# Kernel tuning notes

Measured on AMD Instinct MI355X. Metric: run time of the kernel, lower is better.

Reference implementation:

```python
import jax, jax.numpy as jnp
import numpy as np

B, C, H, W = 32, 1536, 14, 14   # input is (B*4, C, H, W); joint -> (B, C, 2H, 2W)
CI = C // 2                     # non-local inter_channels
EPS = 1e-5


def conv1x1(x, w, b):
    # x: (b, cin, h, w); w: (cout, cin); b: (cout,)
    return jnp.einsum('bchw,oc->bohw', x, w) + b[None, :, None, None]


def maxpool2(x):
    b, c, h, w = x.shape
    return x.reshape(b, c, h // 2, 2, w // 2, 2).max(axis=(3, 5))


def setup_inputs():
    key = jax.random.key(0)
    ks = jax.random.split(key, 12)
    s = 0.02
    return {
        'x': jax.random.normal(ks[0], (B * 4, C, H, W), jnp.float32),
        'w_theta': jax.random.normal(ks[1], (CI, C), jnp.float32) * s,
        'b_theta': jnp.zeros((CI,), jnp.float32),
        'w_phi': jax.random.normal(ks[2], (CI, C), jnp.float32) * s,
        'b_phi': jnp.zeros((CI,), jnp.float32),
        'w_g': jax.random.normal(ks[3], (CI, C), jnp.float32) * s,
        'b_g': jnp.zeros((CI,), jnp.float32),
        'w_W': jax.random.normal(ks[4], (C, CI), jnp.float32) * s,
        'b_W': jnp.zeros((C,), jnp.float32),
        'bn_gamma': jax.random.normal(ks[5], (C,), jnp.float32) * 0.1 + 1.0,
        'bn_beta': jax.random.normal(ks[6], (C,), jnp.float32) * 0.1,
        'bn_mean': jax.random.normal(ks[7], (C,), jnp.float32) * 0.1,
        'bn_var': jnp.ones((C,), jnp.float32),
    }


def joint(x):
    # (B*4, C, H, W) -> (B, C, 2H, 2W): 4 views tiled in a 2x2 grid
    x4 = x.reshape(B, 4, C, H, W)
    top = jnp.concatenate([x4[:, 0], x4[:, 1]], axis=-1)   # (B, C, H, 2W)
    bot = jnp.concatenate([x4[:, 2], x4[:, 3]], axis=-1)
    return jnp.concatenate([top, bot], axis=-2)             # (B, C, 2H, 2W)


def reference(x, w_theta, b_theta, w_phi, b_phi, w_g, b_g, w_W, b_W,
              bn_gamma, bn_beta, bn_mean, bn_var):
    xj = joint(x)                                           # (B, C, Hj, Wj)
    b, c, hj, wj = xj.shape
    n = hj * wj                                             # 784 query positions

    theta = conv1x1(xj, w_theta, b_theta).reshape(b, CI, n)             # (B, CI, N)
    phi = maxpool2(conv1x1(xj, w_phi, b_phi)).reshape(b, CI, -1)        # (B, CI, N/4)
    g = maxpool2(conv1x1(xj, w_g, b_g)).reshape(b, CI, -1)              # (B, CI, N/4)

    f = jnp.einsum('bcn,bcm->bnm', theta, phi)              # (B, N, N/4)
    attn = jax.nn.softmax(f, axis=-1)
    y = jnp.einsum('bnm,bcm->bcn', attn, g)                 # (B, CI, N)
    y = y.reshape(b, CI, hj, wj)

    w_y = conv1x1(y, w_W, b_W)
    # BatchNorm (inference form)
    inv = jax.lax.rsqrt(bn_var + EPS)
    w_y = (w_y - bn_mean[None, :, None, None]) * (bn_gamma * inv)[None, :, None, None] \
          + bn_beta[None, :, None, None]
    return w_y + xj
```

## Files before the change

### kernel.cpp

```cpp
#include <hip/hip_runtime.h>
#include <hip/hip_bf16.h>

typedef __attribute__((ext_vector_type(8))) _Float16 f16x8;
typedef __attribute__((ext_vector_type(4))) float f32x4;
typedef __attribute__((ext_vector_type(4))) unsigned short us4;
typedef __attribute__((ext_vector_type(8))) unsigned short us8;

#define B_   32
#define C_   1536
#define CI_  768
#define N_   784
#define S_   196
#define MP_  224
#define MK_  196

__device__ __forceinline__ unsigned short f2h(float f) {
    _Float16 h = (_Float16)f;
    return __builtin_bit_cast(unsigned short, h);
}
__device__ __forceinline__ f32x4 mfma_f16(f16x8 a, f16x8 b, f32x4 c) {
    return __builtin_amdgcn_mfma_f32_16x16x32_f16(a, b, c, 0, 0, 0);
}
__device__ __forceinline__ void gl_lds16(const unsigned short* g, unsigned short* l) {
    __builtin_amdgcn_global_load_lds(
        (const __attribute__((address_space(1))) unsigned int*)g,
        (__attribute__((address_space(3))) unsigned int*)l, 16, 0, 0);
}

__device__ __forceinline__ void stage24(const unsigned short* Arow,
                                        const unsigned short* Brow,
                                        unsigned short* A_s, unsigned short* B_s,
                                        int k0, int stride,
                                        int wv, int l4r, int l4c_sw) {
    for (int c = wv; c < 24; c += 4) {
        if (c < 16) {
            gl_lds16(Arow + (size_t)(c * 16 + l4r) * stride + k0 + l4c_sw * 8,
                     A_s + c * 512);
        } else {
            int cb = c - 16;
            gl_lds16(Brow + (size_t)(cb * 16 + l4r) * stride + k0 + l4c_sw * 8,
                     B_s + cb * 512);
        }
    }
}

#define PIPE_WAIT_BARRIER()                                   \
    do {                                                      \
        asm volatile("s_waitcnt vmcnt(6)" ::: "memory");      \
        __builtin_amdgcn_s_barrier();                         \
        __builtin_amdgcn_sched_barrier(0);                    \
    } while (0)

__global__ __launch_bounds__(256) void k_cvt(const float* __restrict__ src,
                                             unsigned short* __restrict__ dst,
                                             int count4) {
    int idx = blockIdx.x * 256 + threadIdx.x;
    if (idx < count4) {
        f32x4 v = ((const f32x4*)src)[idx];
        us4 o;
        o[0] = f2h(v[0]); o[1] = f2h(v[1]); o[2] = f2h(v[2]); o[3] = f2h(v[3]);
        ((us4*)dst)[idx] = o;
    }
}

__global__ __launch_bounds__(256) void k_build_xjT(const float* __restrict__ x,
                                                   unsigned short* __restrict__ xjT) {
    __shared__ __align__(16) unsigned short lds[196 * 40];
    int c0 = blockIdx.x * 32;
    int b4 = blockIdx.y;
    int b = b4 >> 2, v = b4 & 3;
    int tid = threadIdx.x;
    const float* src = x + ((size_t)b4 * C_ + c0) * S_;
    for (int idx = tid; idx < 32 * 49; idx += 256) {
        int cl = idx / 49;
        int sq = idx - cl * 49;
        f32x4 val = *(const f32x4*)(src + (size_t)cl * S_ + sq * 4);
        int s = sq * 4;
        lds[(s + 0) * 40 + cl] = f2h(val[0]);
        lds[(s + 1) * 40 + cl] = f2h(val[1]);
        lds[(s + 2) * 40 + cl] = f2h(val[2]);
        lds[(s + 3) * 40 + cl] = f2h(val[3]);
    }
    __syncthreads();
    int rowbase = (v >> 1) * 14, colbase = (v & 1) * 14;
    for (int idx = tid; idx < 196 * 4; idx += 256) {
        int s = idx >> 2, ch = idx & 3;
        int hh = s / 14, ww = s - hh * 14;
        int n = (rowbase + hh) * 28 + colbase + ww;
        us8 val = *(const us8*)(&lds[s * 40 + ch * 8]);
        *(us8*)(xjT + ((size_t)b * N_ + n) * C_ + c0 + ch * 8) = val;
    }
}

__global__ __launch_bounds__(256) void k_bnprep(const float* __restrict__ bw,
                                                const float* __restrict__ gamma,
                                                const float* __restrict__ beta,
                                                const float* __restrict__ mean,
                                                const float* __restrict__ var,
                                                float* __restrict__ scale,
                                                float* __restrict__ shift) {
    int i = blockIdx.x * 256 + threadIdx.x;
    if (i < C_) {
        float sc = gamma[i] * rsqrtf(var[i] + 1e-5f);
        scale[i] = sc;
        shift[i] = (bw[i] - mean[i]) * sc + beta[i];
    }
}

#define COMPUTE_STEP4(As, Bs)                                                     \
    {                                                                             \
        __builtin_amdgcn_s_setprio(1);                                            \
        f16x8 a0_ = *(const f16x8*)(&(As)[((wv * 4 + 0) * 16 + lr) * 32 + rcol]); \
        f16x8 a1_ = *(const f16x8*)(&(As)[((wv * 4 + 1) * 16 + lr) * 32 + rcol]); \
        f16x8 a2_ = *(const f16x8*)(&(As)[((wv * 4 + 2) * 16 + lr) * 32 + rcol]); \
        f16x8 a3_ = *(const f16x8*)(&(As)[((wv * 4 + 3) * 16 + lr) * 32 + rcol]); \
        _Pragma("unroll")                                                         \
        for (int j = 0; j < 7; ++j) {                                             \
            f16x8 bb = *(const f16x8*)(&(Bs)[(j * 16 + lr) * 32 + rcol]);         \
            acc[0][j] = mfma_f16(a0_, bb, acc[0][j]);                             \
            acc[1][j] = mfma_f16(a1_, bb, acc[1][j]);                             \
            acc[2][j] = mfma_f16(a2_, bb, acc[2][j]);                             \
            acc[3][j] = mfma_f16(a3_, bb, acc[3][j]);                             \
        }                                                                         \
        __builtin_amdgcn_s_setprio(0);                                            \
    }

__global__ __launch_bounds__(256, 2) void k_conv3(
    const unsigned short* __restrict__ xjT,
    const unsigned short* __restrict__ wf,
    const float* __restrict__ b_theta, const float* __restrict__ b_phi,
    const float* __restrict__ b_g,
    unsigned short* __restrict__ theta_T, unsigned short* __restrict__ phi_p,
    unsigned short* __restrict__ g_p) {
    __shared__ __align__(16) unsigned char smem[73728];
    unsigned short* A0 = (unsigned short*)smem;
    unsigned short* B0 = A0 + 8192;
    unsigned short* A1 = A0 + 12288;
    unsigned short* B1 = A0 + 20480;
    unsigned short* A2 = A0 + 24576;
    unsigned short* B2 = A0 + 32768;
    float* fLDS = (float*)smem;

    int tn = blockIdx.x;
    int tm = blockIdx.y;
    int b  = blockIdx.z;
    int o0 = tm * 256, n0 = tn * 112;
    int region = o0 / 768;
    int obase = o0 - region * 768;
    const float* bias = (region == 0) ? b_theta : (region == 1) ? b_phi : b_g;

    int tid = threadIdx.x;
    int wv = tid >> 6, lane = tid & 63, lr = lane & 15, quad = lane >> 4;
    int l4r = lane >> 2, l4c = lane & 3;
    int l4c_sw = l4c ^ ((l4r >> 1) & 3);
    int rcol = (quad ^ ((lr >> 1) & 3)) * 8;

    f32x4 acc[4][7];
#pragma unroll
    for (int i = 0; i < 4; ++i)
#pragma unroll
        for (int j = 0; j < 7; ++j) acc[i][j] = (f32x4){0.f, 0.f, 0.f, 0.f};

    const unsigned short* Arow = wf + (size_t)o0 * C_;
    const unsigned short* Brow = xjT + ((size_t)b * N_ + n0) * C_;

    stage24(Arow, Brow, A0, B0, 0, C_, wv, l4r, l4c_sw);
    stage24(Arow, Brow, A1, B1, 32, C_, wv, l4r, l4c_sw);
    for (int kk = 0; kk < 48; kk += 3) {
        PIPE_WAIT_BARRIER();
        stage24(Arow, Brow, A2, B2, (kk + 2 < 48 ? kk + 2 : 47) * 32, C_, wv, l4r, l4c_sw);
        COMPUTE_STEP4(A0, B0);
        PIPE_WAIT_BARRIER();
        stage24(Arow, Brow, A0, B0, (kk + 3 < 48 ? kk + 3 : 47) * 32, C_, wv, l4r, l4c_sw);
        COMPUTE_STEP4(A1, B1);
        PIPE_WAIT_BARRIER();
        stage24(Arow, Brow, A1, B1, (kk + 4 < 48 ? kk + 4 : 47) * 32, C_, wv, l4r, l4c_sw);
        COMPUTE_STEP4(A2, B2);
    }
    asm volatile("s_waitcnt vmcnt(0)" ::: "memory");
    __syncthreads();

    for (int h = 0; h < 4; ++h) {
        if (wv == h) {
#pragma unroll
            for (int i = 0; i < 4; ++i)
#pragma unroll
                for (int j = 0; j < 7; ++j)
#pragma unroll
                    for (int r = 0; r < 4; ++r) {
                        int o_rel = i * 16 + quad * 4 + r;
                        int n_l = j * 16 + lr;
                        fLDS[o_rel * 112 + n_l] = acc[i][j][r];
                    }
        }
        __syncthreads();
        if (region == 0) {
            for (int idx = tid; idx < 112 * 8; idx += 256) {
                int n_l = idx >> 3, ch = idx & 7;
                us8 outv;
#pragma unroll
                for (int k = 0; k < 8; ++k) {
                    int o_rel = ch * 8 + k;
                    float val = fLDS[o_rel * 112 + n_l] + bias[obase + h * 64 + o_rel];
                    outv[k] = f2h(val);
                }
                *(us8*)(theta_T + ((size_t)b * N_ + n0 + n_l) * CI_ + o0 + h * 64 + ch * 8) = outv;
            }
        } else if (region == 1) {
            for (int idx = tid; idx < 28 * 8; idx += 256) {
                int mm = idx >> 3, ch = idx & 7;
                int a = mm / 14, mw = mm - a * 14;
                int m = (tn * 2 + a) * 14 + mw;
                int sb = a * 56 + mw * 2;
                us8 outv;
#pragma unroll
                for (int k = 0; k < 8; ++k) {
                    int o_rel = ch * 8 + k;
                    const float* p = &fLDS[o_rel * 112 + sb];
                    float val = fmaxf(fmaxf(p[0], p[1]), fmaxf(p[28], p[29]));
                    val += bias[obase + h * 64 + o_rel];
                    outv[k] = f2h(val);
                }
                *(us8*)(phi_p + ((size_t)b * MP_ + m) * CI_ + obase + h * 64 + ch * 8) = outv;
            }
        } else {
            for (int idx = tid; idx < 128; idx += 256) {
                int o_rel = idx >> 1, a = idx & 1;
                int ci = obase + h * 64 + o_rel;
                unsigned short* dst = g_p + ((size_t)b * CI_ + ci) * MP_ + (tn * 2 + a) * 14;
                const float* p0 = &fLDS[o_rel * 112 + a * 56];
                float bv = bias[obase + h * 64 + o_rel];
#pragma unroll
                for (int mw = 0; mw < 14; ++mw) {
                    const float* p = p0 + mw * 2;
                    dst[mw] = f2h(fmaxf(fmaxf(p[0], p[1]), fmaxf(p[28], p[29])) + bv);
                }
            }
        }
        __syncthreads();
    }
}

__global__ __launch_bounds__(256) void k_attn(
    const unsigned short* __restrict__ theta_T,
    const unsigned short* __restrict__ phi_p,
    const unsigned short* __restrict__ g_p,
    unsigned short* __restrict__ y) {
    __shared__ __align__(16) float f_s[32 * 228];

    int nb = blockIdx.x, b = blockIdx.y;
    int n0 = nb * 32;
    int tid = threadIdx.x, wv = tid >> 6, lane = tid & 63, lr = lane & 15, quad = lane >> 4;
    int mf0 = wv * 4;
    int nm = (mf0 + 4 <= 14) ? 4 : (14 - mf0);

    int na0 = n0 + lr;       if (na0 > 783) na0 = 783;
    int na1 = n0 + 16 + lr;  if (na1 > 783) na1 = 783;
    const unsigned short* tA0 = theta_T + ((size_t)b * N_ + na0) * CI_ + quad * 8;
    const unsigned short* tA1 = theta_T + ((size_t)b * N_ + na1) * CI_ + quad * 8;

    f32x4 acc[2][4];
#pragma unroll
    for (int i = 0; i < 2; ++i)
#pragma unroll
        for (int j = 0; j < 4; ++j) acc[i][j] = (f32x4){0.f, 0.f, 0.f, 0.f};

    for (int kk = 0; kk < 24; ++kk) {
        int k0 = kk * 32;
        f16x8 a0 = *(const f16x8*)(tA0 + k0);
        f16x8 a1 = *(const f16x8*)(tA1 + k0);
        for (int j = 0; j < nm; ++j) {
            f16x8 bb = *(const f16x8*)(phi_p +
                ((size_t)b * MP_ + (mf0 + j) * 16 + lr) * CI_ + k0 + quad * 8);
            acc[0][j] = mfma_f16(a0, bb, acc[0][j]);
            acc[1][j] = mfma_f16(a1, bb, acc[1][j]);
        }
    }
    for (int i = 0; i < 2; ++i)
        for (int j = 0; j < nm; ++j)
#pragma unroll
            for (int r = 0; r < 4; ++r)
                f_s[(i * 16 + quad * 4 + r) * 228 + (mf0 + j) * 16 + lr] = acc[i][j][r];
    __syncthreads();
    {
        int row = tid >> 3, sub = tid & 7;
        float* rowp = f_s + row * 228;
        int m0 = sub * 28;
        float mx = -1e30f;
#pragma unroll
        for (int m = 0; m < 28; ++m)
            if (m0 + m < MK_) mx = fmaxf(mx, rowp[m0 + m]);
        mx = fmaxf(mx, __shfl_xor(mx, 1));
        mx = fmaxf(mx, __shfl_xor(mx, 2));
        mx = fmaxf(mx, __shfl_xor(mx, 4));
        float sum = 0.f;
#pragma unroll
        for (int m = 0; m < 28; ++m) {
            float e = (m0 + m < MK_) ? __expf(rowp[m0 + m] - mx) : 0.f;
            rowp[m0 + m] = e;
            sum += e;
        }
        sum += __shfl_xor(sum, 1);
        sum += __shfl_xor(sum, 2);
        sum += __shfl_xor(sum, 4);
        float inv = 1.0f / sum;
#pragma unroll
        for (int m = 0; m < 28; ++m) rowp[m0 + m] *= inv;
    }
    __syncthreads();
    for (int c3 = 0; c3 < 3; ++c3) {
        int ci0 = c3 * 256;
        f32x4 acc2[2][4];
#pragma unroll
        for (int i = 0; i < 2; ++i)
#pragma unroll
            for (int j = 0; j < 4; ++j) acc2[i][j] = (f32x4){0.f, 0.f, 0.f, 0.f};
        for (int km = 0; km < 7; ++km) {
            int k0 = km * 32;
            f16x8 a[2];
#pragma unroll
            for (int i = 0; i < 2; ++i) {
                const float* fp = &f_s[(i * 16 + lr) * 228 + k0 + quad * 8];
                f16x8 t;
#pragma unroll
                for (int j = 0; j < 8; ++j) t[j] = (_Float16)fp[j];
                a[i] = t;
            }
#pragma unroll
            for (int j = 0; j < 4; ++j) {
                f16x8 bb = *(const f16x8*)(g_p +
                    ((size_t)b * CI_ + ci0 + (wv * 4 + j) * 16 + lr) * MP_ + k0 + quad * 8);
                acc2[0][j] = mfma_f16(a[0], bb, acc2[0][j]);
                acc2[1][j] = mfma_f16(a[1], bb, acc2[1][j]);
            }
        }
#pragma unroll
        for (int i = 0; i < 2; ++i)
#pragma unroll
            for (int j = 0; j < 4; ++j)
#pragma unroll
                for (int r = 0; r < 4; ++r) {
                    int n = n0 + i * 16 + quad * 4 + r;
                    if (n < N_) {
                        int ci = ci0 + (wv * 4 + j) * 16 + lr;
                        y[((size_t)b * N_ + n) * CI_ + ci] = f2h(acc2[i][j][r]);
                    }
                }
    }
}

__global__ __launch_bounds__(256, 2) void k_final(
    const unsigned short* __restrict__ yb,
    const unsigned short* __restrict__ wfW,
    const float* __restrict__ scale, const float* __restrict__ shift,
    const float* __restrict__ x,
    float* __restrict__ out) {
    __shared__ __align__(16) unsigned short smem_us[36864];
    unsigned short* A0 = smem_us;
    unsigned short* B0 = smem_us + 8192;
    unsigned short* A1 = smem_us + 12288;
    unsigned short* B1 = smem_us + 20480;
    unsigned short* A2 = smem_us + 24576;
    unsigned short* B2 = smem_us + 32768;
    int tn = blockIdx.x, tm = blockIdx.y, b = blockIdx.z;
    int o0 = tm * 256, n0 = tn * 112;
    int tid = threadIdx.x, wv = tid >> 6, lane = tid & 63, lr = lane & 15, quad = lane >> 4;
    int l4r = lane >> 2, l4c = lane & 3;
    int l4c_sw = l4c ^ ((l4r >> 1) & 3);
    int rcol = (quad ^ ((lr >> 1) & 3)) * 8;

    f32x4 acc[4][7];
#pragma unroll
    for (int i = 0; i < 4; ++i)
#pragma unroll
        for (int j = 0; j < 7; ++j) acc[i][j] = (f32x4){0.f, 0.f, 0.f, 0.f};

    const unsigned short* Arow = wfW + (size_t)o0 * CI_;
    const unsigned short* Brow = yb + ((size_t)b * N_ + n0) * CI_;

    stage24(Arow, Brow, A0, B0, 0, CI_, wv, l4r, l4c_sw);
    stage24(Arow, Brow, A1, B1, 32, CI_, wv, l4r, l4c_sw);
    for (int kk = 0; kk < 24; kk += 3) {
        PIPE_WAIT_BARRIER();
        stage24(Arow, Brow, A2, B2, (kk + 2 < 24 ? kk + 2 : 23) * 32, CI_, wv, l4r, l4c_sw);
        COMPUTE_STEP4(A0, B0);
        PIPE_WAIT_BARRIER();
        stage24(Arow, Brow, A0, B0, (kk + 3 < 24 ? kk + 3 : 23) * 32, CI_, wv, l4r, l4c_sw);
        COMPUTE_STEP4(A1, B1);
        PIPE_WAIT_BARRIER();
        stage24(Arow, Brow, A1, B1, (kk + 4 < 24 ? kk + 4 : 23) * 32, CI_, wv, l4r, l4c_sw);
        COMPUTE_STEP4(A2, B2);
    }
    asm volatile("s_waitcnt vmcnt(0)" ::: "memory");
    __syncthreads();
#pragma unroll
    for (int i = 0; i < 4; ++i)
#pragma unroll
        for (int r = 0; r < 4; ++r) {
            int o = o0 + (wv * 4 + i) * 16 + quad * 4 + r;
            float sc = scale[o], sh = shift[o];
#pragma unroll
            for (int j = 0; j < 7; ++j) {
                int n = n0 + j * 16 + lr;
                int hh = n / 28, ww = n - hh * 28;
                int vv = ((hh >= 14) ? 2 : 0) + ((ww >= 14) ? 1 : 0);
                int s = (hh - ((hh >= 14) ? 14 : 0)) * 14 + (ww - ((ww >= 14) ? 14 : 0));
                float xval = x[((size_t)(b * 4 + vv) * C_ + o) * S_ + s];
                out[((size_t)b * C_ + o) * N_ + n] = acc[i][j][r] * sc + sh + xval;
            }
        }
}

extern "C" void kernel_launch(void* const* d_in, const int* in_sizes, int n_in,
                              void* d_out, int out_size, void* d_ws, size_t ws_size,
                              hipStream_t stream) {
    (void)in_sizes; (void)n_in; (void)out_size; (void)ws_size;
    const float* x       = (const float*)d_in[0];
    const float* w_theta = (const float*)d_in[1];
    const float* b_theta = (const float*)d_in[2];
    const float* w_phi   = (const float*)d_in[3];
    const float* b_phi   = (const float*)d_in[4];
    const float* w_g     = (const float*)d_in[5];
    const float* b_g     = (const float*)d_in[6];
    const float* w_W     = (const float*)d_in[7];
    const float* b_W     = (const float*)d_in[8];
    const float* gamma   = (const float*)d_in[9];
    const float* beta    = (const float*)d_in[10];
    const float* mean    = (const float*)d_in[11];
    const float* var     = (const float*)d_in[12];

    char* ob = (char*)d_out;
    unsigned short* xjT     = (unsigned short*)(ob);
    unsigned short* theta_T = (unsigned short*)(ob + 77070336);
    unsigned short* phi_p   = (unsigned short*)(ob + 115605504);
    unsigned short* g_p     = (unsigned short*)(ob + 126615552);
    unsigned short* wf3     = (unsigned short*)(ob + 137625600);

    char* ws = (char*)d_ws;
    unsigned short* yb    = (unsigned short*)(ws);
    unsigned short* wfW   = (unsigned short*)(ws + 38535168);
    float*          scale = (float*)(ws + 40894464);
    float*          shift = (float*)(ws + 40900608);

    hipMemsetAsync(phi_p, 0, 11010048, stream);
    hipMemsetAsync(g_p, 0, 11010048, stream);

    k_bnprep<<<6, 256, 0, stream>>>(b_W, gamma, beta, mean, var, scale, shift);
    k_cvt<<<1152, 256, 0, stream>>>(w_theta, wf3,                294912);
    k_cvt<<<1152, 256, 0, stream>>>(w_phi,   wf3 + 768 * 1536,   294912);
    k_cvt<<<1152, 256, 0, stream>>>(w_g,     wf3 + 2 * 768 * 1536, 294912);
    k_cvt<<<1152, 256, 0, stream>>>(w_W,     wfW,                294912);
    k_build_xjT<<<dim3(48, 128), 256, 0, stream>>>(x, xjT);
    k_conv3<<<dim3(7, 9, 32), 256, 0, stream>>>(xjT, wf3, b_theta, b_phi, b_g,
                                                theta_T, phi_p, g_p);
    k_attn<<<dim3(25, 32), 256, 0, stream>>>(theta_T, phi_p, g_p, yb);
    k_final<<<dim3(7, 6, 32), 256, 0, stream>>>(yb, wfW, scale, shift, x,
                                                (float*)d_out);
}
```

Before: 796.7 us.

## Double-buffer conv3 for higher occupancy and remap blocks across XCDs

k_conv3 goes from a triple-buffered async pipeline to a two-stage double buffer. It drops the unused 24th B chunk, cutting LDS to 46KB so launch bounds can rise to 3 blocks per CU, and it removes the setprio hints. All three main kernels now launch on a flat 1D grid with an XCD-aware index remap, so blocks sharing a batch or weight tile land on the same XCD and can reuse its L2. Only k_final keeps the prioritized compute step. The trade-off is less prefetch depth and plain __syncthreads barriers in conv3, which may expose more load latency, and the 3-per-CU bound may force register spills.

```diff
diff --git a/kernel.cpp b/kernel.cpp
--- a/kernel.cpp
+++ b/kernel.cpp
@@ -25,6 +25,23 @@
     __builtin_amdgcn_global_load_lds(
         (const __attribute__((address_space(1))) unsigned int*)g,
         (__attribute__((address_space(3))) unsigned int*)l, 16, 0, 0);
+}
+
+__device__ __forceinline__ void stage23(const unsigned short* Arow,
+                                        const unsigned short* Brow,
+                                        unsigned short* A_s, unsigned short* B_s,
+                                        int k0, int stride,
+                                        int wv, int l4r, int l4c_sw) {
+    for (int c = wv; c < 23; c += 4) {
+        if (c < 16) {
+            gl_lds16(Arow + (size_t)(c * 16 + l4r) * stride + k0 + l4c_sw * 8,
+                     A_s + c * 512);
+        } else {
+            int cb = c - 16;
+            gl_lds16(Brow + (size_t)(cb * 16 + l4r) * stride + k0 + l4c_sw * 8,
+                     B_s + cb * 512);
+        }
+    }
 }
 
 __device__ __forceinline__ void stage24(const unsigned short* Arow,
@@ -109,7 +126,6 @@
 
 #define COMPUTE_STEP4(As, Bs)                                                     \
     {                                                                             \
-        __builtin_amdgcn_s_setprio(1);                                            \
         f16x8 a0_ = *(const f16x8*)(&(As)[((wv * 4 + 0) * 16 + lr) * 32 + rcol]); \
         f16x8 a1_ = *(const f16x8*)(&(As)[((wv * 4 + 1) * 16 + lr) * 32 + rcol]); \
         f16x8 a2_ = *(const f16x8*)(&(As)[((wv * 4 + 2) * 16 + lr) * 32 + rcol]); \
@@ -122,28 +138,35 @@
             acc[2][j] = mfma_f16(a2_, bb, acc[2][j]);                             \
             acc[3][j] = mfma_f16(a3_, bb, acc[3][j]);                             \
         }                                                                         \
+    }
+
+#define COMPUTE_STEP4P(As, Bs)                                                    \
+    {                                                                             \
+        __builtin_amdgcn_s_setprio(1);                                            \
+        COMPUTE_STEP4(As, Bs);                                                    \
         __builtin_amdgcn_s_setprio(0);                                            \
     }
 
-__global__ __launch_bounds__(256, 2) void k_conv3(
+__global__ __launch_bounds__(256, 3) void k_conv3(
     const unsigned short* __restrict__ xjT,
     const unsigned short* __restrict__ wf,
     const float* __restrict__ b_theta, const float* __restrict__ b_phi,
     const float* __restrict__ b_g,
     unsigned short* __restrict__ theta_T, unsigned short* __restrict__ phi_p,
     unsigned short* __restrict__ g_p) {
-    __shared__ __align__(16) unsigned char smem[73728];
+    __shared__ __align__(16) unsigned char smem[47104];
     unsigned short* A0 = (unsigned short*)smem;
     unsigned short* B0 = A0 + 8192;
-    unsigned short* A1 = A0 + 12288;
-    unsigned short* B1 = A0 + 20480;
-    unsigned short* A2 = A0 + 24576;
-    unsigned short* B2 = A0 + 32768;
+    unsigned short* A1 = A0 + 11776;
+    unsigned short* B1 = A0 + 19968;
     float* fLDS = (float*)smem;
 
-    int tn = blockIdx.x;
-    int tm = blockIdx.y;
-    int b  = blockIdx.z;
+    int f = blockIdx.x;
+    int xcd = f & 7, g = f >> 3;
+    int pg = g / 9, tm = g - pg * 9;
+    int pair = xcd * 28 + pg;
+    int tn = pair % 7, b = pair / 7;
+
     int o0 = tm * 256, n0 = tn * 112;
     int region = o0 / 768;
     int obase = o0 - region * 768;
@@ -164,21 +187,17 @@
     const unsigned short* Arow = wf + (size_t)o0 * C_;
     const unsigned short* Brow = xjT + ((size_t)b * N_ + n0) * C_;
 
-    stage24(Arow, Brow, A0, B0, 0, C_, wv, l4r, l4c_sw);
-    stage24(Arow, Brow, A1, B1, 32, C_, wv, l4r, l4c_sw);
-    for (int kk = 0; kk < 48; kk += 3) {
-        PIPE_WAIT_BARRIER();
-        stage24(Arow, Brow, A2, B2, (kk + 2 < 48 ? kk + 2 : 47) * 32, C_, wv, l4r, l4c_sw);
+    stage23(Arow, Brow, A0, B0, 0, C_, wv, l4r, l4c_sw);
+    __syncthreads();
+    for (int kk = 0; kk < 48; kk += 2) {
+        stage23(Arow, Brow, A1, B1, (kk + 1) * 32, C_, wv, l4r, l4c_sw);
         COMPUTE_STEP4(A0, B0);
-        PIPE_WAIT_BARRIER();
-        stage24(Arow, Brow, A0, B0, (kk + 3 < 48 ? kk + 3 : 47) * 32, C_, wv, l4r, l4c_sw);
+        __syncthreads();
+        if (kk + 2 < 48)
+            stage23(Arow, Brow, A0, B0, (kk + 2) * 32, C_, wv, l4r, l4c_sw);
         COMPUTE_STEP4(A1, B1);
-        PIPE_WAIT_BARRIER();
-        stage24(Arow, Brow, A1, B1, (kk + 4 < 48 ? kk + 4 : 47) * 32, C_, wv, l4r, l4c_sw);
-        COMPUTE_STEP4(A2, B2);
-    }
-    asm volatile("s_waitcnt vmcnt(0)" ::: "memory");
-    __syncthreads();
+        __syncthreads();
+    }
 
     for (int h = 0; h < 4; ++h) {
         if (wv == h) {
@@ -248,7 +267,10 @@
     unsigned short* __restrict__ y) {
     __shared__ __align__(16) float f_s[32 * 228];
 
-    int nb = blockIdx.x, b = blockIdx.y;
+    int f = blockIdx.x;
+    int xcd = f & 7, g = f >> 3;
+    int idx2 = xcd * 100 + g;
+    int b = idx2 / 25, nb = idx2 - b * 25;
     int n0 = nb * 32;
     int tid = threadIdx.x, wv = tid >> 6, lane = tid & 63, lr = lane & 15, quad = lane >> 4;
     int mf0 = wv * 4;
@@ -362,7 +384,13 @@
     unsigned short* B1 = smem_us + 20480;
     unsigned short* A2 = smem_us + 24576;
     unsigned short* B2 = smem_us + 32768;
-    int tn = blockIdx.x, tm = blockIdx.y, b = blockIdx.z;
+
+    int f = blockIdx.x;
+    int xcd = f & 7, g = f >> 3;
+    int pg = g / 6, tm = g - pg * 6;
+    int pair = xcd * 28 + pg;
+    int tn = pair % 7, b = pair / 7;
+
     int o0 = tm * 256, n0 = tn * 112;
     int tid = threadIdx.x, wv = tid >> 6, lane = tid & 63, lr = lane & 15, quad = lane >> 4;
     int l4r = lane >> 2, l4c = lane & 3;
@@ -383,13 +411,13 @@
     for (int kk = 0; kk < 24; kk += 3) {
         PIPE_WAIT_BARRIER();
         stage24(Arow, Brow, A2, B2, (kk + 2 < 24 ? kk + 2 : 23) * 32, CI_, wv, l4r, l4c_sw);
-        COMPUTE_STEP4(A0, B0);
+        COMPUTE_STEP4P(A0, B0);
         PIPE_WAIT_BARRIER();
         stage24(Arow, Brow, A0, B0, (kk + 3 < 24 ? kk + 3 : 23) * 32, CI_, wv, l4r, l4c_sw);
-        COMPUTE_STEP4(A1, B1);
+        COMPUTE_STEP4P(A1, B1);
         PIPE_WAIT_BARRIER();
         stage24(Arow, Brow, A1, B1, (kk + 4 < 24 ? kk + 4 : 23) * 32, CI_, wv, l4r, l4c_sw);
-        COMPUTE_STEP4(A2, B2);
+        COMPUTE_STEP4P(A2, B2);
     }
     asm volatile("s_waitcnt vmcnt(0)" ::: "memory");
     __syncthreads();
@@ -451,9 +479,9 @@
     k_cvt<<<1152, 256, 0, stream>>>(w_g,     wf3 + 2 * 768 * 1536, 294912);
     k_cvt<<<1152, 256, 0, stream>>>(w_W,     wfW,                294912);
     k_build_xjT<<<dim3(48, 128), 256, 0, stream>>>(x, xjT);
-    k_conv3<<<dim3(7, 9, 32), 256, 0, stream>>>(xjT, wf3, b_theta, b_phi, b_g,
-                                                theta_T, phi_p, g_p);
-    k_attn<<<dim3(25, 32), 256, 0, stream>>>(theta_T, phi_p, g_p, yb);
-    k_final<<<dim3(7, 6, 32), 256, 0, stream>>>(yb, wfW, scale, shift, x,
-                                                (float*)d_out);
-}
+    k_conv3<<<2016, 256, 0, stream>>>(xjT, wf3, b_theta, b_phi, b_g,
+                                      theta_T, phi_p, g_p);
+    k_attn<<<800, 256, 0, stream>>>(theta_T, phi_p, g_p, yb);
+    k_final<<<1344, 256, 0, stream>>>(yb, wfW, scale, shift, x,
+                                      (float*)d_out);
+}
```

After: 756.8 us. 1.05x faster.
